# Optimization experiments

Measured on AMD Instinct MI355X. Metric: run time of the kernel, lower is better.

The kernel has to match this reference:

```python
import jax, jax.numpy as jnp
import numpy as np
from jax import lax

B, T, C = 4, 2048, 1024
E, DFF, TOPK = 8, 4096, 2


def setup_inputs() -> dict:
    key = jax.random.key(0)
    ks = jax.random.split(key, 5)
    scale = 0.02
    x = jax.random.normal(ks[0], (B, T, C), dtype=jnp.float32)
    router_w = jax.random.normal(ks[1], (C, E), dtype=jnp.float32) * scale
    router_b = jnp.zeros((E,), dtype=jnp.float32)
    w1 = jax.random.normal(ks[2], (E, C, DFF), dtype=jnp.float32) * scale
    b1 = jnp.zeros((E, DFF), dtype=jnp.float32)
    w2 = jax.random.normal(ks[3], (E, DFF, C), dtype=jnp.float32) * scale
    b2 = jnp.zeros((E, C), dtype=jnp.float32)
    return {"x": x, "router_w": router_w, "router_b": router_b,
            "w1": w1, "b1": b1, "w2": w2, "b2": b2, "top_k": TOPK}


def reference(x, router_w, router_b, w1, b1, w2, b2, top_k):
    # Router: softmax then top-k (matches torch.topk(F.softmax(logits)))
    logits = jnp.einsum('btc,ce->bte', x, router_w) + router_b   # [B,T,E]
    probs = jax.nn.softmax(logits, axis=-1)
    weights, indices = lax.top_k(probs, top_k)                    # [B,T,k]
    n_exp = w1.shape[0]
    # Combined per-expert weight per token (sum over top-k slots hitting expert j)
    onehot = jax.nn.one_hot(indices, n_exp, dtype=x.dtype)        # [B,T,k,E]
    cw = jnp.sum(weights[..., None] * onehot, axis=-2)            # [B,T,E]
    bsz, seq, dim = x.shape
    flat_x = x.reshape(-1, dim)                                   # [N,C]
    flat_cw = cw.reshape(-1, n_exp)                               # [N,E]
    out = jnp.zeros_like(flat_x)
    for j in range(n_exp):  # fixed small expert loop (dropout=0 -> eval)
        h = jax.nn.gelu(flat_x @ w1[j] + b1[j], approximate=False)
        out = out + flat_cw[:, j:j + 1] * (h @ w2[j] + b2[j])
    return out.reshape(bsz, seq, dim)
```

## Files before the change

### kernel.cpp

```cpp
#include <hip/hip_runtime.h>
#include <math.h>

typedef __bf16 bf16;
typedef bf16 bf16x4 __attribute__((ext_vector_type(4)));
typedef bf16 bf16x8 __attribute__((ext_vector_type(8)));
typedef float f32x4 __attribute__((ext_vector_type(4)));

#define NTOK 8192
#define CDIM 1024
#define EXP 8
#define DFF 4096
#define BM 128
#define BN 128
#define BK 32

__device__ __forceinline__ void gld_lds16(const bf16* g, bf16* l) {
  __builtin_amdgcn_global_load_lds(
      (const __attribute__((address_space(1))) unsigned int*)g,
      (__attribute__((address_space(3))) unsigned int*)l, 16, 0, 0);
}

__global__ __launch_bounds__(256) void convert_x(const float* __restrict__ in,
                                                 bf16* __restrict__ out) {
  int idx = (blockIdx.x * 256 + threadIdx.x) * 8;
  float4 a = *(const float4*)(in + idx);
  float4 b = *(const float4*)(in + idx + 4);
  bf16x8 v;
  v[0] = (bf16)a.x; v[1] = (bf16)a.y; v[2] = (bf16)a.z; v[3] = (bf16)a.w;
  v[4] = (bf16)b.x; v[5] = (bf16)b.y; v[6] = (bf16)b.z; v[7] = (bf16)b.w;
  *(bf16x8*)(out + idx) = v;
}

__global__ __launch_bounds__(256) void transpose_cvt(
    const float* __restrict__ in, bf16* __restrict__ out, int R, int Cin) {
  __shared__ float tile[32][33];
  int e = blockIdx.z;
  const float* ip = in + (size_t)e * R * Cin;
  bf16* op = out + (size_t)e * R * Cin;
  int c0 = blockIdx.x * 32, r0 = blockIdx.y * 32;
  int tx = threadIdx.x & 31, ty = threadIdx.x >> 5;
#pragma unroll
  for (int i = 0; i < 4; i++)
    tile[ty + 8 * i][tx] = ip[(size_t)(r0 + ty + 8 * i) * Cin + c0 + tx];
  __syncthreads();
  int c = threadIdx.x >> 3, r4 = (threadIdx.x & 7) * 4;
  bf16x4 v;
  v[0] = (bf16)tile[r4][c];
  v[1] = (bf16)tile[r4 + 1][c];
  v[2] = (bf16)tile[r4 + 2][c];
  v[3] = (bf16)tile[r4 + 3][c];
  *(bf16x4*)&op[(size_t)(c0 + c) * R + r0 + r4] = v;
}

__global__ __launch_bounds__(256) void router_kernel(
    const float* __restrict__ x, const float* __restrict__ rw,
    const float* __restrict__ rb, unsigned int* __restrict__ cnt,
    int* __restrict__ list, float* __restrict__ wq) {
  int wave = threadIdx.x >> 6, lane = threadIdx.x & 63;
  int t = blockIdx.x * 4 + wave;
  if (t >= NTOK) return;
  const float* xr = x + (size_t)t * CDIM;
  float acc[8] = {0.f, 0.f, 0.f, 0.f, 0.f, 0.f, 0.f, 0.f};
  for (int c = lane; c < CDIM; c += 64) {
    float xv = xr[c];
    const float4* rp = (const float4*)(rw + c * 8);
    float4 r0 = rp[0], r1 = rp[1];
    acc[0] += xv * r0.x; acc[1] += xv * r0.y;
    acc[2] += xv * r0.z; acc[3] += xv * r0.w;
    acc[4] += xv * r1.x; acc[5] += xv * r1.y;
    acc[6] += xv * r1.z; acc[7] += xv * r1.w;
  }
#pragma unroll
  for (int e = 0; e < 8; e++)
#pragma unroll
    for (int off = 32; off; off >>= 1) acc[e] += __shfl_down(acc[e], off);
  if (lane == 0) {
    float p[8], mx = -1e30f;
#pragma unroll
    for (int e = 0; e < 8; e++) { p[e] = acc[e] + rb[e]; mx = fmaxf(mx, p[e]); }
    float s = 0.f;
#pragma unroll
    for (int e = 0; e < 8; e++) { p[e] = expf(p[e] - mx); s += p[e]; }
    float inv = 1.0f / s;
#pragma unroll
    for (int e = 0; e < 8; e++) p[e] *= inv;
    int i1 = 0;
#pragma unroll
    for (int e = 1; e < 8; e++) if (p[e] > p[i1]) i1 = e;
    int i2 = (i1 == 0) ? 1 : 0;
#pragma unroll
    for (int e = 0; e < 8; e++) if (e != i1 && p[e] > p[i2]) i2 = e;
    unsigned s0 = atomicAdd(&cnt[i1], 1u);
    list[i1 * NTOK + s0] = t * 2;
    unsigned s1 = atomicAdd(&cnt[i2], 1u);
    list[i2 * NTOK + s1] = t * 2 + 1;
    wq[t * 2] = p[i1];
    wq[t * 2 + 1] = p[i2];
  }
}

__global__ __launch_bounds__(256) void gemm1_kernel(
    const bf16* __restrict__ xb, const bf16* __restrict__ w1b,
    const float* __restrict__ b1, const int* __restrict__ list,
    const unsigned int* __restrict__ cnt, bf16* __restrict__ h) {
  int e = blockIdx.z;
  int count = (int)min(cnt[e], (unsigned)NTOK);
  int m0 = blockIdx.y * BM;
  if (m0 >= count) return;
  int n0 = blockIdx.x * BN;

  __shared__ __align__(16) bf16 As[BM][BK];
  __shared__ __align__(16) bf16 Bs[BN][BK];
  __shared__ int Ls[BM];

  int tid = threadIdx.x;
  if (tid < BM) {
    int gi = m0 + tid;
    Ls[tid] = (gi < count) ? list[e * NTOK + gi] : 0;
  }
  __syncthreads();

  const bf16* arow0 = xb + (size_t)(Ls[tid >> 2] >> 1) * CDIM + (tid & 3) * 8;
  const bf16* arow1 =
      xb + (size_t)(Ls[64 + (tid >> 2)] >> 1) * CDIM + (tid & 3) * 8;
  bf16* adst0 = &As[tid >> 2][(tid & 3) * 8];
  bf16* adst1 = &As[64 + (tid >> 2)][(tid & 3) * 8];
  const bf16* brow0 = w1b + (size_t)e * DFF * CDIM +
                      (size_t)(n0 + (tid >> 2)) * CDIM + (tid & 3) * 8;
  const bf16* brow1 = brow0 + (size_t)64 * CDIM;
  bf16* bdst0 = &Bs[tid >> 2][(tid & 3) * 8];
  bf16* bdst1 = &Bs[64 + (tid >> 2)][(tid & 3) * 8];

  f32x4 acc[4][4] = {};
  int wave = tid >> 6, lane = tid & 63;
  int wm = wave & 1, wn = wave >> 1;
  int ln = lane & 15, kq = lane >> 4;

  for (int k0 = 0; k0 < CDIM; k0 += BK) {
    __syncthreads();
    gld_lds16(arow0 + k0, adst0);
    gld_lds16(arow1 + k0, adst1);
    gld_lds16(brow0 + k0, bdst0);
    gld_lds16(brow1 + k0, bdst1);
    __syncthreads();
    bf16x8 af[4], bfr[4];
#pragma unroll
    for (int i = 0; i < 4; i++)
      af[i] = *(bf16x8*)&As[wm * 64 + i * 16 + ln][kq * 8];
#pragma unroll
    for (int j = 0; j < 4; j++)
      bfr[j] = *(bf16x8*)&Bs[wn * 64 + j * 16 + ln][kq * 8];
#pragma unroll
    for (int i = 0; i < 4; i++)
#pragma unroll
      for (int j = 0; j < 4; j++)
        acc[i][j] = __builtin_amdgcn_mfma_f32_16x16x32_bf16(af[i], bfr[j],
                                                            acc[i][j], 0, 0, 0);
  }
#pragma unroll
  for (int j = 0; j < 4; j++) {
    int n = n0 + wn * 64 + j * 16 + ln;
    float b1v = b1[e * DFF + n];
#pragma unroll
    for (int i = 0; i < 4; i++) {
#pragma unroll
      for (int r = 0; r < 4; r++) {
        int mrow = wm * 64 + i * 16 + kq * 4 + r;
        if (m0 + mrow < count) {
          int enc = Ls[mrow];
          float v = acc[i][j][r] + b1v;
          float g = 0.5f * v * (1.0f + erff(v * 0.70710678118654752f));
          h[(size_t)enc * DFF + n] = (bf16)g;
        }
      }
    }
  }
}

__global__ __launch_bounds__(256) void gemm2_kernel(
    const bf16* __restrict__ h, const bf16* __restrict__ w2b,
    const float* __restrict__ b2, const int* __restrict__ list,
    const unsigned int* __restrict__ cnt, const float* __restrict__ wq,
    float* __restrict__ out) {
  int e = blockIdx.z;
  int count = (int)min(cnt[e], (unsigned)NTOK);
  int m0 = blockIdx.y * BM;
  if (m0 >= count) return;
  int n0 = blockIdx.x * BN;

  __shared__ __align__(16) bf16 As[BM][BK];
  __shared__ __align__(16) bf16 Bs[BN][BK];
  __shared__ int Ls[BM];

  int tid = threadIdx.x;
  if (tid < BM) {
    int gi = m0 + tid;
    Ls[tid] = (gi < count) ? list[e * NTOK + gi] : 0;
  }
  __syncthreads();

  const bf16* arow0 = h + (size_t)Ls[tid >> 2] * DFF + (tid & 3) * 8;
  const bf16* arow1 = h + (size_t)Ls[64 + (tid >> 2)] * DFF + (tid & 3) * 8;
  bf16* adst0 = &As[tid >> 2][(tid & 3) * 8];
  bf16* adst1 = &As[64 + (tid >> 2)][(tid & 3) * 8];
  const bf16* brow0 = w2b + (size_t)e * CDIM * DFF +
                      (size_t)(n0 + (tid >> 2)) * DFF + (tid & 3) * 8;
  const bf16* brow1 = brow0 + (size_t)64 * DFF;
  bf16* bdst0 = &Bs[tid >> 2][(tid & 3) * 8];
  bf16* bdst1 = &Bs[64 + (tid >> 2)][(tid & 3) * 8];

  f32x4 acc[4][4] = {};
  int wave = tid >> 6, lane = tid & 63;
  int wm = wave & 1, wn = wave >> 1;
  int ln = lane & 15, kq = lane >> 4;

  for (int k0 = 0; k0 < DFF; k0 += BK) {
    __syncthreads();
    gld_lds16(arow0 + k0, adst0);
    gld_lds16(arow1 + k0, adst1);
    gld_lds16(brow0 + k0, bdst0);
    gld_lds16(brow1 + k0, bdst1);
    __syncthreads();
    bf16x8 af[4], bfr[4];
#pragma unroll
    for (int i = 0; i < 4; i++)
      af[i] = *(bf16x8*)&As[wm * 64 + i * 16 + ln][kq * 8];
#pragma unroll
    for (int j = 0; j < 4; j++)
      bfr[j] = *(bf16x8*)&Bs[wn * 64 + j * 16 + ln][kq * 8];
#pragma unroll
    for (int i = 0; i < 4; i++)
#pragma unroll
      for (int j = 0; j < 4; j++)
        acc[i][j] = __builtin_amdgcn_mfma_f32_16x16x32_bf16(af[i], bfr[j],
                                                            acc[i][j], 0, 0, 0);
  }
#pragma unroll
  for (int j = 0; j < 4; j++) {
    int n = n0 + wn * 64 + j * 16 + ln;
    float b2v = b2[e * CDIM + n];
#pragma unroll
    for (int i = 0; i < 4; i++) {
#pragma unroll
      for (int r = 0; r < 4; r++) {
        int mrow = wm * 64 + i * 16 + kq * 4 + r;
        if (m0 + mrow < count) {
          int enc = Ls[mrow];
          int t = enc >> 1;
          float w = wq[enc];
          atomicAdd(&out[(size_t)t * CDIM + n], w * (acc[i][j][r] + b2v));
        }
      }
    }
  }
}

extern "C" void kernel_launch(void* const* d_in, const int* in_sizes, int n_in,
                              void* d_out, int out_size, void* d_ws,
                              size_t ws_size, hipStream_t stream) {
  const float* x = (const float*)d_in[0];
  const float* rw = (const float*)d_in[1];
  const float* rb = (const float*)d_in[2];
  const float* w1 = (const float*)d_in[3];
  const float* b1 = (const float*)d_in[4];
  const float* w2 = (const float*)d_in[5];
  const float* b2 = (const float*)d_in[6];
  float* out = (float*)d_out;

  char* ws = (char*)d_ws;
  size_t o = 0;
  auto carve = [&](size_t bytes) {
    void* p = ws + o;
    o = (o + bytes + 255) & ~(size_t)255;
    return p;
  };
  bf16* w1b = (bf16*)carve((size_t)EXP * DFF * CDIM * 2);
  bf16* w2b = (bf16*)carve((size_t)EXP * DFF * CDIM * 2);
  bf16* h = (bf16*)carve((size_t)2 * NTOK * DFF * 2);
  bf16* xb = (bf16*)carve((size_t)NTOK * CDIM * 2);
  int* list = (int*)carve((size_t)EXP * NTOK * 4);
  float* wq = (float*)carve((size_t)2 * NTOK * 4);
  unsigned int* cnt = (unsigned int*)carve(64);

  hipMemsetAsync(out, 0, (size_t)out_size * sizeof(float), stream);
  hipMemsetAsync(cnt, 0, 64, stream);

  convert_x<<<NTOK * CDIM / (256 * 8), 256, 0, stream>>>(x, xb);
  transpose_cvt<<<dim3(DFF / 32, CDIM / 32, EXP), 256, 0, stream>>>(w1, w1b,
                                                                    CDIM, DFF);
  transpose_cvt<<<dim3(CDIM / 32, DFF / 32, EXP), 256, 0, stream>>>(w2, w2b,
                                                                    DFF, CDIM);
  router_kernel<<<NTOK / 4, 256, 0, stream>>>(x, rw, rb, cnt, list, wq);
  gemm1_kernel<<<dim3(DFF / BN, NTOK / BM, EXP), 256, 0, stream>>>(
      xb, w1b, b1, list, cnt, h);
  gemm2_kernel<<<dim3(CDIM / BN, NTOK / BM, EXP), 256, 0, stream>>>(
      h, w2b, b2, list, cnt, wq, out);
}
```

Measured before the change: 1.176 ms.

## Double-buffer LDS tiles in both GEMMs and split-K the second GEMM

Both expert GEMMs now use two LDS buffers, so the global-to-LDS load of the next K tile is issued before the MFMAs on the current tile, with one barrier per iteration instead of two. The second GEMM also splits its K dimension (DFF) into two halves across extra grid blocks. Partial results are accumulated with the existing atomics, and the bias is added only by the first split. This adds more blocks to the N=1024 GEMM, which has few tiles per expert, at the cost of twice as many atomic adds to the output and twice the LDS per block.

Measured after the change: 1.198 ms. No clear change (+1.8%).

```diff
diff --git a/kernel.cpp b/kernel.cpp
--- a/kernel.cpp
+++ b/kernel.cpp
@@ -13,6 +13,7 @@
 #define BM 128
 #define BN 128
 #define BK 32
+#define KSPLIT 2
 
 __device__ __forceinline__ void gld_lds16(const bf16* g, bf16* l) {
   __builtin_amdgcn_global_load_lds(
@@ -109,8 +110,8 @@
   if (m0 >= count) return;
   int n0 = blockIdx.x * BN;
 
-  __shared__ __align__(16) bf16 As[BM][BK];
-  __shared__ __align__(16) bf16 Bs[BN][BK];
+  __shared__ __align__(16) bf16 As[2][BM][BK];
+  __shared__ __align__(16) bf16 Bs[2][BN][BK];
   __shared__ int Ls[BM];
 
   int tid = threadIdx.x;
@@ -123,39 +124,47 @@
   const bf16* arow0 = xb + (size_t)(Ls[tid >> 2] >> 1) * CDIM + (tid & 3) * 8;
   const bf16* arow1 =
       xb + (size_t)(Ls[64 + (tid >> 2)] >> 1) * CDIM + (tid & 3) * 8;
-  bf16* adst0 = &As[tid >> 2][(tid & 3) * 8];
-  bf16* adst1 = &As[64 + (tid >> 2)][(tid & 3) * 8];
   const bf16* brow0 = w1b + (size_t)e * DFF * CDIM +
                       (size_t)(n0 + (tid >> 2)) * CDIM + (tid & 3) * 8;
   const bf16* brow1 = brow0 + (size_t)64 * CDIM;
-  bf16* bdst0 = &Bs[tid >> 2][(tid & 3) * 8];
-  bf16* bdst1 = &Bs[64 + (tid >> 2)][(tid & 3) * 8];
+  int soff = (tid >> 2) * BK + (tid & 3) * 8;
+  bf16* adst[2] = {&As[0][0][0] + soff, &As[1][0][0] + soff};
+  bf16* bdst[2] = {&Bs[0][0][0] + soff, &Bs[1][0][0] + soff};
 
   f32x4 acc[4][4] = {};
   int wave = tid >> 6, lane = tid & 63;
   int wm = wave & 1, wn = wave >> 1;
   int ln = lane & 15, kq = lane >> 4;
 
-  for (int k0 = 0; k0 < CDIM; k0 += BK) {
-    __syncthreads();
-    gld_lds16(arow0 + k0, adst0);
-    gld_lds16(arow1 + k0, adst1);
-    gld_lds16(brow0 + k0, bdst0);
-    gld_lds16(brow1 + k0, bdst1);
-    __syncthreads();
+  const int NIT = CDIM / BK;
+  gld_lds16(arow0, adst[0]);
+  gld_lds16(arow1, adst[0] + 64 * BK);
+  gld_lds16(brow0, bdst[0]);
+  gld_lds16(brow1, bdst[0] + 64 * BK);
+  __syncthreads();
+  for (int it = 0; it < NIT; it++) {
+    int cur = it & 1;
+    if (it + 1 < NIT) {
+      int kn = (it + 1) * BK;
+      gld_lds16(arow0 + kn, adst[cur ^ 1]);
+      gld_lds16(arow1 + kn, adst[cur ^ 1] + 64 * BK);
+      gld_lds16(brow0 + kn, bdst[cur ^ 1]);
+      gld_lds16(brow1 + kn, bdst[cur ^ 1] + 64 * BK);
+    }
     bf16x8 af[4], bfr[4];
 #pragma unroll
     for (int i = 0; i < 4; i++)
-      af[i] = *(bf16x8*)&As[wm * 64 + i * 16 + ln][kq * 8];
+      af[i] = *(bf16x8*)&As[cur][wm * 64 + i * 16 + ln][kq * 8];
 #pragma unroll
     for (int j = 0; j < 4; j++)
-      bfr[j] = *(bf16x8*)&Bs[wn * 64 + j * 16 + ln][kq * 8];
+      bfr[j] = *(bf16x8*)&Bs[cur][wn * 64 + j * 16 + ln][kq * 8];
 #pragma unroll
     for (int i = 0; i < 4; i++)
 #pragma unroll
       for (int j = 0; j < 4; j++)
         acc[i][j] = __builtin_amdgcn_mfma_f32_16x16x32_bf16(af[i], bfr[j],
                                                             acc[i][j], 0, 0, 0);
+    __syncthreads();
   }
 #pragma unroll
   for (int j = 0; j < 4; j++) {
@@ -182,14 +191,17 @@
     const float* __restrict__ b2, const int* __restrict__ list,
     const unsigned int* __restrict__ cnt, const float* __restrict__ wq,
     float* __restrict__ out) {
-  int e = blockIdx.z;
+  int e = blockIdx.z >> 1;
+  int ks = blockIdx.z & (KSPLIT - 1);
   int count = (int)min(cnt[e], (unsigned)NTOK);
   int m0 = blockIdx.y * BM;
   if (m0 >= count) return;
   int n0 = blockIdx.x * BN;
-
-  __shared__ __align__(16) bf16 As[BM][BK];
-  __shared__ __align__(16) bf16 Bs[BN][BK];
+  const int KCH = DFF / KSPLIT;
+  int kbase = ks * KCH;
+
+  __shared__ __align__(16) bf16 As[2][BM][BK];
+  __shared__ __align__(16) bf16 Bs[2][BN][BK];
   __shared__ int Ls[BM];
 
   int tid = threadIdx.x;
@@ -199,46 +211,56 @@
   }
   __syncthreads();
 
-  const bf16* arow0 = h + (size_t)Ls[tid >> 2] * DFF + (tid & 3) * 8;
-  const bf16* arow1 = h + (size_t)Ls[64 + (tid >> 2)] * DFF + (tid & 3) * 8;
-  bf16* adst0 = &As[tid >> 2][(tid & 3) * 8];
-  bf16* adst1 = &As[64 + (tid >> 2)][(tid & 3) * 8];
+  const bf16* arow0 =
+      h + (size_t)Ls[tid >> 2] * DFF + kbase + (tid & 3) * 8;
+  const bf16* arow1 =
+      h + (size_t)Ls[64 + (tid >> 2)] * DFF + kbase + (tid & 3) * 8;
   const bf16* brow0 = w2b + (size_t)e * CDIM * DFF +
-                      (size_t)(n0 + (tid >> 2)) * DFF + (tid & 3) * 8;
+                      (size_t)(n0 + (tid >> 2)) * DFF + kbase + (tid & 3) * 8;
   const bf16* brow1 = brow0 + (size_t)64 * DFF;
-  bf16* bdst0 = &Bs[tid >> 2][(tid & 3) * 8];
-  bf16* bdst1 = &Bs[64 + (tid >> 2)][(tid & 3) * 8];
+  int soff = (tid >> 2) * BK + (tid & 3) * 8;
+  bf16* adst[2] = {&As[0][0][0] + soff, &As[1][0][0] + soff};
+  bf16* bdst[2] = {&Bs[0][0][0] + soff, &Bs[1][0][0] + soff};
 
   f32x4 acc[4][4] = {};
   int wave = tid >> 6, lane = tid & 63;
   int wm = wave & 1, wn = wave >> 1;
   int ln = lane & 15, kq = lane >> 4;
 
-  for (int k0 = 0; k0 < DFF; k0 += BK) {
-    __syncthreads();
-    gld_lds16(arow0 + k0, adst0);
-    gld_lds16(arow1 + k0, adst1);
-    gld_lds16(brow0 + k0, bdst0);
-    gld_lds16(brow1 + k0, bdst1);
-    __syncthreads();
+  const int NIT = KCH / BK;
+  gld_lds16(arow0, adst[0]);
+  gld_lds16(arow1, adst[0] + 64 * BK);
+  gld_lds16(brow0, bdst[0]);
+  gld_lds16(brow1, bdst[0] + 64 * BK);
+  __syncthreads();
+  for (int it = 0; it < NIT; it++) {
+    int cur = it & 1;
+    if (it + 1 < NIT) {
+      int kn = (it + 1) * BK;
+      gld_lds16(arow0 + kn, adst[cur ^ 1]);
+      gld_lds16(arow1 + kn, adst[cur ^ 1] + 64 * BK);
+      gld_lds16(brow0 + kn, bdst[cur ^ 1]);
+      gld_lds16(brow1 + kn, bdst[cur ^ 1] + 64 * BK);
+    }
     bf16x8 af[4], bfr[4];
 #pragma unroll
     for (int i = 0; i < 4; i++)
-      af[i] = *(bf16x8*)&As[wm * 64 + i * 16 + ln][kq * 8];
+      af[i] = *(bf16x8*)&As[cur][wm * 64 + i * 16 + ln][kq * 8];
 #pragma unroll
     for (int j = 0; j < 4; j++)
-      bfr[j] = *(bf16x8*)&Bs[wn * 64 + j * 16 + ln][kq * 8];
+      bfr[j] = *(bf16x8*)&Bs[cur][wn * 64 + j * 16 + ln][kq * 8];
 #pragma unroll
     for (int i = 0; i < 4; i++)
 #pragma unroll
       for (int j = 0; j < 4; j++)
         acc[i][j] = __builtin_amdgcn_mfma_f32_16x16x32_bf16(af[i], bfr[j],
                                                             acc[i][j], 0, 0, 0);
+    __syncthreads();
   }
 #pragma unroll
   for (int j = 0; j < 4; j++) {
     int n = n0 + wn * 64 + j * 16 + ln;
-    float b2v = b2[e * CDIM + n];
+    float b2v = (ks == 0) ? b2[e * CDIM + n] : 0.0f;
 #pragma unroll
     for (int i = 0; i < 4; i++) {
 #pragma unroll
@@ -293,6 +315,6 @@
   router_kernel<<<NTOK / 4, 256, 0, stream>>>(x, rw, rb, cnt, list, wq);
   gemm1_kernel<<<dim3(DFF / BN, NTOK / BM, EXP), 256, 0, stream>>>(
       xb, w1b, b1, list, cnt, h);
-  gemm2_kernel<<<dim3(CDIM / BN, NTOK / BM, EXP), 256, 0, stream>>>(
+  gemm2_kernel<<<dim3(CDIM / BN, NTOK / BM, EXP * KSPLIT), 256, 0, stream>>>(
       h, w2b, b2, list, cnt, wq, out);
 }
```
